# Performance work log

Measured on AMD Instinct MI355X. Metric: run time of the kernel, lower is better.

## Reference

```python
import jax, jax.numpy as jnp
import numpy as np

N = 4096
IN_DIM, HID, OUT_DIM = 512, 256, 128
GAMMA = 6.0            # MCP weight truncation: w(y) = max(1 - y/gamma, 0)
LAM_HAT = 0.9
LAM = 1.0 / LAM_HAT - 1.0
PROP_STEPS = 10


def setup_inputs() -> dict:
    key = jax.random.key(0)
    k_a, k_f, k_w1, k_b1, k_w2, k_b2 = jax.random.split(key, 6)
    p = 32.0 / N  # avg degree ~32
    U = jax.random.uniform(k_a, (N, N))
    A = (U < p).astype(jnp.float32)
    A = jnp.maximum(A, A.T)                       # symmetric
    A = A * (1.0 - jnp.eye(N, dtype=jnp.float32))  # zero diagonal (loops added in forward)
    F = jax.random.normal(k_f, (N, IN_DIM), dtype=jnp.float32)
    W1 = jax.random.normal(k_w1, (IN_DIM, HID), dtype=jnp.float32) * 0.05
    b1 = jax.random.normal(k_b1, (HID,), dtype=jnp.float32) * 0.01
    W2 = jax.random.normal(k_w2, (HID, OUT_DIM), dtype=jnp.float32) * 0.05
    b2 = jax.random.normal(k_b2, (OUT_DIM,), dtype=jnp.float32) * 0.01
    return {"A": A, "F": F, "W1": W1, "b1": b1, "W2": W2, "b2": b2}


def reference(A, F, W1, b1, W2, b2):
    n = A.shape[0]
    # MLP (eval mode: dropout off)
    F0 = jnp.maximum(F @ W1 + b1, 0.0) @ W2 + b2          # [N, out_dim]
    # add self loops
    A = A + jnp.eye(n, dtype=A.dtype)
    D = A.sum(-1)                                          # [N]
    D_sq = jnp.sqrt(D)[:, None]                            # [N,1]
    A_t = A / (D_sq * D_sq.T)                              # sym-normalized adjacency
    diag = jnp.arange(n)
    Fc = F0
    for _ in range(PROP_STEPS):
        X = Fc / D_sq                                      # [N, d]
        sq = jnp.sum(X * X, axis=-1)                       # [N]
        Z = sq[:, None] + sq[None, :] - 2.0 * (X @ X.T)    # pairwise squared dist [N,N]
        Z = jax.lax.stop_gradient(jnp.maximum(Z, 0.0))
        Wm = jnp.maximum(1.0 - jnp.sqrt(Z) / GAMMA, 0.0)   # MCP IRLS weight
        Wm = Wm.at[diag, diag].set(0.0)
        Wm = jnp.where(jnp.isnan(Wm), 1.0, Wm)
        # quasi-Newton IRLS step
        Q = ((Wm * A).sum(-1) / D + LAM)[:, None]          # [N,1]
        Fc = (Wm * A_t) @ Fc / Q + LAM * F0 / Q
    return Fc
```

## Files before the change

kernel.cpp:

```cpp
#include <hip/hip_runtime.h>

#define NN 4096
#define IN_DIM 512
#define HID 256
#define OUT_DIM 128
#define MAXDEG 192
#define INV_GAMMA (1.0f / 6.0f)
#define LAM 0.11111111111111116f
#define PROP_STEPS 10

__global__ void k_analyze(const float* __restrict__ A, unsigned short* __restrict__ cols,
                          int* __restrict__ deg, float* __restrict__ DsqInv,
                          float* __restrict__ Dinv) {
    int wid = threadIdx.x >> 6, lane = threadIdx.x & 63;
    int row = blockIdx.x * 4 + wid;
    const float4* Ar = (const float4*)(A + (size_t)row * NN);
    unsigned short* crow = cols + (size_t)row * MAXDEG;
    int cnt = 0;
    float fsum = 0.f;
    for (int it = 0; it < NN / 256; ++it) {
        float4 v = Ar[it * 64 + lane];
        fsum += (v.x + v.y) + (v.z + v.w);
        int colbase = (it * 64 + lane) * 4;
        float comp[4] = {v.x, v.y, v.z, v.w};
#pragma unroll
        for (int c = 0; c < 4; ++c) {
            bool nz = (comp[c] != 0.f);
            unsigned long long m = __ballot(nz);
            if (nz) {
                int off = cnt + __popcll(m & ((1ull << lane) - 1ull));
                if (off < MAXDEG) crow[off] = (unsigned short)(colbase + c);
            }
            cnt += __popcll(m);
        }
    }
#pragma unroll
    for (int m = 1; m < 64; m <<= 1) fsum += __shfl_xor(fsum, m);
    if (lane == 0) {
        float D = fsum + 1.0f;
        deg[row] = cnt < MAXDEG ? cnt : MAXDEG;
        DsqInv[row] = 1.0f / sqrtf(D);
        Dinv[row] = 1.0f / D;
    }
}

__global__ __launch_bounds__(256) void k_mlp(const float* __restrict__ F,
                      const float* __restrict__ W1, const float* __restrict__ b1,
                      const float* __restrict__ W2, const float* __restrict__ b2,
                      const float* __restrict__ DsqInv,
                      float* __restrict__ F0, float* __restrict__ X0) {
    __shared__ __align__(16) float sF[8 * IN_DIM];
    __shared__ __align__(16) float sW[32 * 256];
    __shared__ __align__(16) float sH[8 * HID];
    int r0 = blockIdx.x * 8;
    int t = threadIdx.x;
#pragma unroll
    for (int i = 0; i < 4; ++i) {
        int idx = i * 256 + t;
        int r = idx >> 7, q = idx & 127;
        *(float4*)&sF[r * IN_DIM + 4 * q] = *(const float4*)&F[(size_t)(r0 + r) * IN_DIM + 4 * q];
    }
    {
        int cq = t & 63, rg = t >> 6;
        float4 accA = make_float4(0.f, 0.f, 0.f, 0.f);
        float4 accB = make_float4(0.f, 0.f, 0.f, 0.f);
        for (int kt = 0; kt < IN_DIM / 32; ++kt) {
            __syncthreads();
#pragma unroll
            for (int i = 0; i < 8; ++i) {
                int idx = i * 256 + t;
                int kr = idx >> 6, q = idx & 63;
                *(float4*)&sW[kr * 256 + 4 * q] =
                    *(const float4*)&W1[(size_t)(kt * 32 + kr) * HID + 4 * q];
            }
            __syncthreads();
#pragma unroll
            for (int kk = 0; kk < 32; ++kk) {
                int k = kt * 32 + kk;
                float4 w = *(float4*)&sW[kk * 256 + 4 * cq];
                float fa = sF[(2 * rg) * IN_DIM + k];
                float fb = sF[(2 * rg + 1) * IN_DIM + k];
                accA.x = fmaf(fa, w.x, accA.x); accA.y = fmaf(fa, w.y, accA.y);
                accA.z = fmaf(fa, w.z, accA.z); accA.w = fmaf(fa, w.w, accA.w);
                accB.x = fmaf(fb, w.x, accB.x); accB.y = fmaf(fb, w.y, accB.y);
                accB.z = fmaf(fb, w.z, accB.z); accB.w = fmaf(fb, w.w, accB.w);
            }
        }
        float4 b = *(const float4*)&b1[4 * cq];
        float4 ha, hb;
        ha.x = fmaxf(accA.x + b.x, 0.f); ha.y = fmaxf(accA.y + b.y, 0.f);
        ha.z = fmaxf(accA.z + b.z, 0.f); ha.w = fmaxf(accA.w + b.w, 0.f);
        hb.x = fmaxf(accB.x + b.x, 0.f); hb.y = fmaxf(accB.y + b.y, 0.f);
        hb.z = fmaxf(accB.z + b.z, 0.f); hb.w = fmaxf(accB.w + b.w, 0.f);
        *(float4*)&sH[(2 * rg) * HID + 4 * cq] = ha;
        *(float4*)&sH[(2 * rg + 1) * HID + 4 * cq] = hb;
    }
    {
        int c = t & 127, half = t >> 7;
        float acc2[4] = {0.f, 0.f, 0.f, 0.f};
        for (int kt = 0; kt < HID / 32; ++kt) {
            __syncthreads();
#pragma unroll
            for (int i = 0; i < 4; ++i) {
                int idx = i * 256 + t;
                int kr = idx >> 5, q = idx & 31;
                *(float4*)&sW[kr * 128 + 4 * q] =
                    *(const float4*)&W2[(size_t)(kt * 32 + kr) * OUT_DIM + 4 * q];
            }
            __syncthreads();
#pragma unroll
            for (int kk = 0; kk < 32; ++kk) {
                int k = kt * 32 + kk;
                float w = sW[kk * 128 + c];
#pragma unroll
                for (int r = 0; r < 4; ++r)
                    acc2[r] = fmaf(sH[(half * 4 + r) * HID + k], w, acc2[r]);
            }
        }
        float b = b2[c];
#pragma unroll
        for (int r = 0; r < 4; ++r) {
            int row = r0 + half * 4 + r;
            float v = acc2[r] + b;
            F0[(size_t)row * OUT_DIM + c] = v;
            X0[(size_t)row * OUT_DIM + c] = v * DsqInv[row];
        }
    }
}

__global__ __launch_bounds__(256) void k_prop(const float* __restrict__ X,
                       const float* __restrict__ F0,
                       const unsigned short* __restrict__ cols, const int* __restrict__ deg,
                       const float* __restrict__ DsqInv, const float* __restrict__ Dinv,
                       float* __restrict__ Xout, float* __restrict__ FcOut, int final_step) {
    __shared__ unsigned short sCols[4][MAXDEG];
    int wid = threadIdx.x >> 6, lane = threadIdx.x & 63;
    int row = blockIdx.x * 4 + wid;
    int g = lane >> 3, oc = lane & 7;
    int dg = deg[row];
    float dsi = DsqInv[row], di = Dinv[row];
    for (int e = lane; e < dg; e += 64) sCols[wid][e] = cols[(size_t)row * MAXDEG + e];
    const float4* Xi4 = (const float4*)(X + (size_t)row * 128 + oc * 16);
    float4 xi0 = Xi4[0], xi1 = Xi4[1], xi2 = Xi4[2], xi3 = Xi4[3];
    float sqi;
    {
        float s = 0.f;
        s = fmaf(xi0.x, xi0.x, s); s = fmaf(xi0.y, xi0.y, s);
        s = fmaf(xi0.z, xi0.z, s); s = fmaf(xi0.w, xi0.w, s);
        s = fmaf(xi1.x, xi1.x, s); s = fmaf(xi1.y, xi1.y, s);
        s = fmaf(xi1.z, xi1.z, s); s = fmaf(xi1.w, xi1.w, s);
        s = fmaf(xi2.x, xi2.x, s); s = fmaf(xi2.y, xi2.y, s);
        s = fmaf(xi2.z, xi2.z, s); s = fmaf(xi2.w, xi2.w, s);
        s = fmaf(xi3.x, xi3.x, s); s = fmaf(xi3.y, xi3.y, s);
        s = fmaf(xi3.z, xi3.z, s); s = fmaf(xi3.w, xi3.w, s);
        s += __shfl_xor(s, 1); s += __shfl_xor(s, 2); s += __shfl_xor(s, 4);
        sqi = s;
    }
    float acc[16];
#pragma unroll
    for (int i = 0; i < 16; ++i) acc[i] = 0.f;
    float qacc = 0.f;
    int nch = (dg + 7) >> 3;
    for (int ch = 0; ch < nch; ++ch) {
        int e = ch * 8 + g;
        bool act = (e < dg);
        int ec = act ? e : (dg - 1);
        int j = (int)sCols[wid][ec];
        const float4* Xj4 = (const float4*)(X + (size_t)j * 128 + oc * 16);
        float4 a = Xj4[0], b = Xj4[1], c = Xj4[2], d = Xj4[3];
        float p = 0.f, sj = 0.f;
        p = fmaf(xi0.x, a.x, p); sj = fmaf(a.x, a.x, sj);
        p = fmaf(xi0.y, a.y, p); sj = fmaf(a.y, a.y, sj);
        p = fmaf(xi0.z, a.z, p); sj = fmaf(a.z, a.z, sj);
        p = fmaf(xi0.w, a.w, p); sj = fmaf(a.w, a.w, sj);
        p = fmaf(xi1.x, b.x, p); sj = fmaf(b.x, b.x, sj);
        p = fmaf(xi1.y, b.y, p); sj = fmaf(b.y, b.y, sj);
        p = fmaf(xi1.z, b.z, p); sj = fmaf(b.z, b.z, sj);
        p = fmaf(xi1.w, b.w, p); sj = fmaf(b.w, b.w, sj);
        p = fmaf(xi2.x, c.x, p); sj = fmaf(c.x, c.x, sj);
        p = fmaf(xi2.y, c.y, p); sj = fmaf(c.y, c.y, sj);
        p = fmaf(xi2.z, c.z, p); sj = fmaf(c.z, c.z, sj);
        p = fmaf(xi2.w, c.w, p); sj = fmaf(c.w, c.w, sj);
        p = fmaf(xi3.x, d.x, p); sj = fmaf(d.x, d.x, sj);
        p = fmaf(xi3.y, d.y, p); sj = fmaf(d.y, d.y, sj);
        p = fmaf(xi3.z, d.z, p); sj = fmaf(d.z, d.z, sj);
        p = fmaf(xi3.w, d.w, p); sj = fmaf(d.w, d.w, sj);
        p += __shfl_xor(p, 1); p += __shfl_xor(p, 2); p += __shfl_xor(p, 4);
        sj += __shfl_xor(sj, 1); sj += __shfl_xor(sj, 2); sj += __shfl_xor(sj, 4);
        float z = fmaxf(sqi + sj - 2.f * p, 0.f);
        float w = fmaxf(1.f - sqrtf(z) * INV_GAMMA, 0.f);
        w = act ? w : 0.f;
        qacc += w;
        acc[0]  = fmaf(w, a.x, acc[0]);  acc[1]  = fmaf(w, a.y, acc[1]);
        acc[2]  = fmaf(w, a.z, acc[2]);  acc[3]  = fmaf(w, a.w, acc[3]);
        acc[4]  = fmaf(w, b.x, acc[4]);  acc[5]  = fmaf(w, b.y, acc[5]);
        acc[6]  = fmaf(w, b.z, acc[6]);  acc[7]  = fmaf(w, b.w, acc[7]);
        acc[8]  = fmaf(w, c.x, acc[8]);  acc[9]  = fmaf(w, c.y, acc[9]);
        acc[10] = fmaf(w, c.z, acc[10]); acc[11] = fmaf(w, c.w, acc[11]);
        acc[12] = fmaf(w, d.x, acc[12]); acc[13] = fmaf(w, d.y, acc[13]);
        acc[14] = fmaf(w, d.z, acc[14]); acc[15] = fmaf(w, d.w, acc[15]);
    }
#pragma unroll
    for (int m = 8; m <= 32; m <<= 1) {
        qacc += __shfl_xor(qacc, m);
#pragma unroll
        for (int i = 0; i < 16; ++i) acc[i] += __shfl_xor(acc[i], m);
    }
    float invQ = 1.f / (qacc * di + LAM);
    if (g == 0) {
        const float4* F04 = (const float4*)(F0 + (size_t)row * 128 + oc * 16);
        float* dstF = (float*)(FcOut + (size_t)row * 128 + oc * 16);
        float* dstX = (float*)(Xout + (size_t)row * 128 + oc * 16);
#pragma unroll
        for (int q = 0; q < 4; ++q) {
            float4 f0 = F04[q];
            float4 o;
            o.x = (dsi * acc[4 * q + 0] + LAM * f0.x) * invQ;
            o.y = (dsi * acc[4 * q + 1] + LAM * f0.y) * invQ;
            o.z = (dsi * acc[4 * q + 2] + LAM * f0.z) * invQ;
            o.w = (dsi * acc[4 * q + 3] + LAM * f0.w) * invQ;
            if (final_step) {
                *(float4*)&dstF[4 * q] = o;
            } else {
                float4 xo;
                xo.x = o.x * dsi; xo.y = o.y * dsi; xo.z = o.z * dsi; xo.w = o.w * dsi;
                *(float4*)&dstX[4 * q] = xo;
            }
        }
    }
}

extern "C" void kernel_launch(void* const* d_in, const int* in_sizes, int n_in,
                              void* d_out, int out_size, void* d_ws, size_t ws_size,
                              hipStream_t stream) {
    const float *A = nullptr, *F = nullptr, *W1 = nullptr, *b1 = nullptr,
                *W2 = nullptr, *b2 = nullptr;
    for (int i = 0; i < n_in; i++) {
        switch (in_sizes[i]) {
            case NN * NN:        A  = (const float*)d_in[i]; break;
            case NN * IN_DIM:    F  = (const float*)d_in[i]; break;
            case IN_DIM * HID:   W1 = (const float*)d_in[i]; break;
            case HID:            b1 = (const float*)d_in[i]; break;
            case HID * OUT_DIM:  W2 = (const float*)d_in[i]; break;
            case OUT_DIM:        b2 = (const float*)d_in[i]; break;
            default: break;
        }
    }
    float* out = (float*)d_out;

    char* ws = (char*)d_ws;
    float* F0     = (float*)ws; ws += (size_t)NN * OUT_DIM * 4;
    float* XA     = (float*)ws; ws += (size_t)NN * OUT_DIM * 4;
    float* XB     = (float*)ws; ws += (size_t)NN * OUT_DIM * 4;
    float* DsqInv = (float*)ws; ws += (size_t)NN * 4;
    float* Dinv   = (float*)ws; ws += (size_t)NN * 4;
    int*   deg    = (int*)ws;   ws += (size_t)NN * 4;
    unsigned short* cols = (unsigned short*)ws; ws += (size_t)NN * MAXDEG * 2;

    hipLaunchKernelGGL(k_analyze, dim3(NN / 4), dim3(256), 0, stream, A, cols, deg, DsqInv, Dinv);
    hipLaunchKernelGGL(k_mlp, dim3(NN / 8), dim3(256), 0, stream,
                       F, W1, b1, W2, b2, DsqInv, F0, XA);

    float* Xc = XA; float* Xn = XB;
    for (int step = 0; step < PROP_STEPS; step++) {
        int fin = (step == PROP_STEPS - 1) ? 1 : 0;
        hipLaunchKernelGGL(k_prop, dim3(NN / 4), dim3(256), 0, stream,
                           Xc, F0, cols, deg, DsqInv, Dinv, Xn, out, fin);
        float* t1 = Xc; Xc = Xn; Xn = t1;
    }
}
```

Measured before the change: 289.8 us.

## Retile MLP with register-prefetched weights and remap prop lanes with gather prefetch

```diff
diff --git a/kernel.cpp b/kernel.cpp
--- a/kernel.cpp
+++ b/kernel.cpp
@@ -49,86 +49,139 @@
                       const float* __restrict__ W2, const float* __restrict__ b2,
                       const float* __restrict__ DsqInv,
                       float* __restrict__ F0, float* __restrict__ X0) {
-    __shared__ __align__(16) float sF[8 * IN_DIM];
+    __shared__ __align__(16) float sF[16 * IN_DIM];
     __shared__ __align__(16) float sW[32 * 256];
-    __shared__ __align__(16) float sH[8 * HID];
-    int r0 = blockIdx.x * 8;
+    __shared__ float sHT[HID * 18];
     int t = threadIdx.x;
-#pragma unroll
-    for (int i = 0; i < 4; ++i) {
+    int r0 = blockIdx.x * 16;
+    const float4* F4 = (const float4*)F;
+    const float4* W1_4 = (const float4*)W1;
+    const float4* W2_4 = (const float4*)W2;
+    float4* sF4 = (float4*)sF;
+    float4* sW4 = (float4*)sW;
+
+#pragma unroll
+    for (int i = 0; i < 8; ++i) {
         int idx = i * 256 + t;
         int r = idx >> 7, q = idx & 127;
-        *(float4*)&sF[r * IN_DIM + 4 * q] = *(const float4*)&F[(size_t)(r0 + r) * IN_DIM + 4 * q];
+        sF4[r * 128 + q] = F4[(size_t)(r0 + r) * 128 + q];
+    }
+    float4 wreg[8];
+#pragma unroll
+    for (int i = 0; i < 8; ++i) {
+        int idx = i * 256 + t;
+        int kr = idx >> 6, q = idx & 63;
+        wreg[i] = W1_4[(size_t)kr * 64 + q];
     }
     {
         int cq = t & 63, rg = t >> 6;
-        float4 accA = make_float4(0.f, 0.f, 0.f, 0.f);
-        float4 accB = make_float4(0.f, 0.f, 0.f, 0.f);
+        float4 acc[4];
+#pragma unroll
+        for (int j = 0; j < 4; ++j) acc[j] = make_float4(0.f, 0.f, 0.f, 0.f);
         for (int kt = 0; kt < IN_DIM / 32; ++kt) {
             __syncthreads();
 #pragma unroll
             for (int i = 0; i < 8; ++i) {
                 int idx = i * 256 + t;
                 int kr = idx >> 6, q = idx & 63;
-                *(float4*)&sW[kr * 256 + 4 * q] =
-                    *(const float4*)&W1[(size_t)(kt * 32 + kr) * HID + 4 * q];
+                sW4[kr * 64 + q] = wreg[i];
             }
             __syncthreads();
-#pragma unroll
-            for (int kk = 0; kk < 32; ++kk) {
-                int k = kt * 32 + kk;
-                float4 w = *(float4*)&sW[kk * 256 + 4 * cq];
-                float fa = sF[(2 * rg) * IN_DIM + k];
-                float fb = sF[(2 * rg + 1) * IN_DIM + k];
-                accA.x = fmaf(fa, w.x, accA.x); accA.y = fmaf(fa, w.y, accA.y);
-                accA.z = fmaf(fa, w.z, accA.z); accA.w = fmaf(fa, w.w, accA.w);
-                accB.x = fmaf(fb, w.x, accB.x); accB.y = fmaf(fb, w.y, accB.y);
-                accB.z = fmaf(fb, w.z, accB.z); accB.w = fmaf(fb, w.w, accB.w);
+            if (kt < IN_DIM / 32 - 1) {
+#pragma unroll
+                for (int i = 0; i < 8; ++i) {
+                    int idx = i * 256 + t;
+                    int kr = idx >> 6, q = idx & 63;
+                    wreg[i] = W1_4[(size_t)((kt + 1) * 32 + kr) * 64 + q];
+                }
+            }
+#pragma unroll
+            for (int g4 = 0; g4 < 8; ++g4) {
+                float4 w0 = sW4[(4 * g4 + 0) * 64 + cq];
+                float4 w1 = sW4[(4 * g4 + 1) * 64 + cq];
+                float4 w2 = sW4[(4 * g4 + 2) * 64 + cq];
+                float4 w3 = sW4[(4 * g4 + 3) * 64 + cq];
+#pragma unroll
+                for (int j = 0; j < 4; ++j) {
+                    float4 f = sF4[(4 * rg + j) * 128 + kt * 8 + g4];
+                    acc[j].x = fmaf(f.x, w0.x, acc[j].x); acc[j].y = fmaf(f.x, w0.y, acc[j].y);
+                    acc[j].z = fmaf(f.x, w0.z, acc[j].z); acc[j].w = fmaf(f.x, w0.w, acc[j].w);
+                    acc[j].x = fmaf(f.y, w1.x, acc[j].x); acc[j].y = fmaf(f.y, w1.y, acc[j].y);
+                    acc[j].z = fmaf(f.y, w1.z, acc[j].z); acc[j].w = fmaf(f.y, w1.w, acc[j].w);
+                    acc[j].x = fmaf(f.z, w2.x, acc[j].x); acc[j].y = fmaf(f.z, w2.y, acc[j].y);
+                    acc[j].z = fmaf(f.z, w2.z, acc[j].z); acc[j].w = fmaf(f.z, w2.w, acc[j].w);
+                    acc[j].x = fmaf(f.w, w3.x, acc[j].x); acc[j].y = fmaf(f.w, w3.y, acc[j].y);
+                    acc[j].z = fmaf(f.w, w3.z, acc[j].z); acc[j].w = fmaf(f.w, w3.w, acc[j].w);
+                }
             }
         }
         float4 b = *(const float4*)&b1[4 * cq];
-        float4 ha, hb;
-        ha.x = fmaxf(accA.x + b.x, 0.f); ha.y = fmaxf(accA.y + b.y, 0.f);
-        ha.z = fmaxf(accA.z + b.z, 0.f); ha.w = fmaxf(accA.w + b.w, 0.f);
-        hb.x = fmaxf(accB.x + b.x, 0.f); hb.y = fmaxf(accB.y + b.y, 0.f);
-        hb.z = fmaxf(accB.z + b.z, 0.f); hb.w = fmaxf(accB.w + b.w, 0.f);
-        *(float4*)&sH[(2 * rg) * HID + 4 * cq] = ha;
-        *(float4*)&sH[(2 * rg + 1) * HID + 4 * cq] = hb;
+#pragma unroll
+        for (int j = 0; j < 4; ++j) {
+            float hx = fmaxf(acc[j].x + b.x, 0.f);
+            float hy = fmaxf(acc[j].y + b.y, 0.f);
+            float hz = fmaxf(acc[j].z + b.z, 0.f);
+            float hw = fmaxf(acc[j].w + b.w, 0.f);
+            int r = 4 * rg + j;
+            sHT[(4 * cq + 0) * 18 + r] = hx;
+            sHT[(4 * cq + 1) * 18 + r] = hy;
+            sHT[(4 * cq + 2) * 18 + r] = hz;
+            sHT[(4 * cq + 3) * 18 + r] = hw;
+        }
+    }
+#pragma unroll
+    for (int i = 0; i < 4; ++i) {
+        int idx = i * 256 + t;
+        int kr = idx >> 5, q = idx & 31;
+        wreg[i] = W2_4[(size_t)kr * 32 + q];
     }
     {
-        int c = t & 127, half = t >> 7;
-        float acc2[4] = {0.f, 0.f, 0.f, 0.f};
+        int cq2 = t & 31, rg2 = t >> 5;
+        float4 accA = make_float4(0.f, 0.f, 0.f, 0.f);
+        float4 accB = make_float4(0.f, 0.f, 0.f, 0.f);
         for (int kt = 0; kt < HID / 32; ++kt) {
             __syncthreads();
 #pragma unroll
             for (int i = 0; i < 4; ++i) {
                 int idx = i * 256 + t;
                 int kr = idx >> 5, q = idx & 31;
-                *(float4*)&sW[kr * 128 + 4 * q] =
-                    *(const float4*)&W2[(size_t)(kt * 32 + kr) * OUT_DIM + 4 * q];
+                sW4[kr * 32 + q] = wreg[i];
             }
             __syncthreads();
+            if (kt < HID / 32 - 1) {
+#pragma unroll
+                for (int i = 0; i < 4; ++i) {
+                    int idx = i * 256 + t;
+                    int kr = idx >> 5, q = idx & 31;
+                    wreg[i] = W2_4[(size_t)((kt + 1) * 32 + kr) * 32 + q];
+                }
+            }
 #pragma unroll
             for (int kk = 0; kk < 32; ++kk) {
-                int k = kt * 32 + kk;
-                float w = sW[kk * 128 + c];
-#pragma unroll
-                for (int r = 0; r < 4; ++r)
-                    acc2[r] = fmaf(sH[(half * 4 + r) * HID + k], w, acc2[r]);
-            }
-        }
-        float b = b2[c];
-#pragma unroll
-        for (int r = 0; r < 4; ++r) {
-            int row = r0 + half * 4 + r;
-            float v = acc2[r] + b;
-            F0[(size_t)row * OUT_DIM + c] = v;
-            X0[(size_t)row * OUT_DIM + c] = v * DsqInv[row];
-        }
+                float4 w = sW4[kk * 32 + cq2];
+                float2 f = *(const float2*)&sHT[(kt * 32 + kk) * 18 + 2 * rg2];
+                accA.x = fmaf(f.x, w.x, accA.x); accA.y = fmaf(f.x, w.y, accA.y);
+                accA.z = fmaf(f.x, w.z, accA.z); accA.w = fmaf(f.x, w.w, accA.w);
+                accB.x = fmaf(f.y, w.x, accB.x); accB.y = fmaf(f.y, w.y, accB.y);
+                accB.z = fmaf(f.y, w.z, accB.z); accB.w = fmaf(f.y, w.w, accB.w);
+            }
+        }
+        float4 b = *(const float4*)&b2[4 * cq2];
+        int rowA = r0 + 2 * rg2, rowB = rowA + 1;
+        float dsA = DsqInv[rowA], dsB = DsqInv[rowB];
+        float4 oA, oB, xA, xB;
+        oA.x = accA.x + b.x; oA.y = accA.y + b.y; oA.z = accA.z + b.z; oA.w = accA.w + b.w;
+        oB.x = accB.x + b.x; oB.y = accB.y + b.y; oB.z = accB.z + b.z; oB.w = accB.w + b.w;
+        xA.x = oA.x * dsA; xA.y = oA.y * dsA; xA.z = oA.z * dsA; xA.w = oA.w * dsA;
+        xB.x = oB.x * dsB; xB.y = oB.y * dsB; xB.z = oB.z * dsB; xB.w = oB.w * dsB;
+        ((float4*)F0)[(size_t)rowA * 32 + cq2] = oA;
+        ((float4*)F0)[(size_t)rowB * 32 + cq2] = oB;
+        ((float4*)X0)[(size_t)rowA * 32 + cq2] = xA;
+        ((float4*)X0)[(size_t)rowB * 32 + cq2] = xB;
     }
 }
 
-__global__ __launch_bounds__(256) void k_prop(const float* __restrict__ X,
+__global__ __launch_bounds__(256, 4) void k_prop(const float* __restrict__ X,
                        const float* __restrict__ F0,
                        const unsigned short* __restrict__ cols, const int* __restrict__ deg,
                        const float* __restrict__ DsqInv, const float* __restrict__ Dinv,
@@ -136,96 +189,93 @@
     __shared__ unsigned short sCols[4][MAXDEG];
     int wid = threadIdx.x >> 6, lane = threadIdx.x & 63;
     int row = blockIdx.x * 4 + wid;
-    int g = lane >> 3, oc = lane & 7;
+    int g = lane >> 4, oc = lane & 15;
     int dg = deg[row];
     float dsi = DsqInv[row], di = Dinv[row];
     for (int e = lane; e < dg; e += 64) sCols[wid][e] = cols[(size_t)row * MAXDEG + e];
-    const float4* Xi4 = (const float4*)(X + (size_t)row * 128 + oc * 16);
-    float4 xi0 = Xi4[0], xi1 = Xi4[1], xi2 = Xi4[2], xi3 = Xi4[3];
+
+    const float4* Xr = (const float4*)(X + (size_t)row * 128);
+    float4 xiA = Xr[oc], xiB = Xr[16 + oc];
     float sqi;
     {
         float s = 0.f;
-        s = fmaf(xi0.x, xi0.x, s); s = fmaf(xi0.y, xi0.y, s);
-        s = fmaf(xi0.z, xi0.z, s); s = fmaf(xi0.w, xi0.w, s);
-        s = fmaf(xi1.x, xi1.x, s); s = fmaf(xi1.y, xi1.y, s);
-        s = fmaf(xi1.z, xi1.z, s); s = fmaf(xi1.w, xi1.w, s);
-        s = fmaf(xi2.x, xi2.x, s); s = fmaf(xi2.y, xi2.y, s);
-        s = fmaf(xi2.z, xi2.z, s); s = fmaf(xi2.w, xi2.w, s);
-        s = fmaf(xi3.x, xi3.x, s); s = fmaf(xi3.y, xi3.y, s);
-        s = fmaf(xi3.z, xi3.z, s); s = fmaf(xi3.w, xi3.w, s);
-        s += __shfl_xor(s, 1); s += __shfl_xor(s, 2); s += __shfl_xor(s, 4);
+        s = fmaf(xiA.x, xiA.x, s); s = fmaf(xiA.y, xiA.y, s);
+        s = fmaf(xiA.z, xiA.z, s); s = fmaf(xiA.w, xiA.w, s);
+        s = fmaf(xiB.x, xiB.x, s); s = fmaf(xiB.y, xiB.y, s);
+        s = fmaf(xiB.z, xiB.z, s); s = fmaf(xiB.w, xiB.w, s);
+        s += __shfl_xor(s, 1); s += __shfl_xor(s, 2);
+        s += __shfl_xor(s, 4); s += __shfl_xor(s, 8);
         sqi = s;
     }
-    float acc[16];
-#pragma unroll
-    for (int i = 0; i < 16; ++i) acc[i] = 0.f;
+    float4 accA = make_float4(0.f, 0.f, 0.f, 0.f);
+    float4 accB = make_float4(0.f, 0.f, 0.f, 0.f);
     float qacc = 0.f;
-    int nch = (dg + 7) >> 3;
-    for (int ch = 0; ch < nch; ++ch) {
-        int e = ch * 8 + g;
-        bool act = (e < dg);
-        int ec = act ? e : (dg - 1);
-        int j = (int)sCols[wid][ec];
-        const float4* Xj4 = (const float4*)(X + (size_t)j * 128 + oc * 16);
-        float4 a = Xj4[0], b = Xj4[1], c = Xj4[2], d = Xj4[3];
-        float p = 0.f, sj = 0.f;
-        p = fmaf(xi0.x, a.x, p); sj = fmaf(a.x, a.x, sj);
-        p = fmaf(xi0.y, a.y, p); sj = fmaf(a.y, a.y, sj);
-        p = fmaf(xi0.z, a.z, p); sj = fmaf(a.z, a.z, sj);
-        p = fmaf(xi0.w, a.w, p); sj = fmaf(a.w, a.w, sj);
-        p = fmaf(xi1.x, b.x, p); sj = fmaf(b.x, b.x, sj);
-        p = fmaf(xi1.y, b.y, p); sj = fmaf(b.y, b.y, sj);
-        p = fmaf(xi1.z, b.z, p); sj = fmaf(b.z, b.z, sj);
-        p = fmaf(xi1.w, b.w, p); sj = fmaf(b.w, b.w, sj);
-        p = fmaf(xi2.x, c.x, p); sj = fmaf(c.x, c.x, sj);
-        p = fmaf(xi2.y, c.y, p); sj = fmaf(c.y, c.y, sj);
-        p = fmaf(xi2.z, c.z, p); sj = fmaf(c.z, c.z, sj);
-        p = fmaf(xi2.w, c.w, p); sj = fmaf(c.w, c.w, sj);
-        p = fmaf(xi3.x, d.x, p); sj = fmaf(d.x, d.x, sj);
-        p = fmaf(xi3.y, d.y, p); sj = fmaf(d.y, d.y, sj);
-        p = fmaf(xi3.z, d.z, p); sj = fmaf(d.z, d.z, sj);
-        p = fmaf(xi3.w, d.w, p); sj = fmaf(d.w, d.w, sj);
-        p += __shfl_xor(p, 1); p += __shfl_xor(p, 2); p += __shfl_xor(p, 4);
-        sj += __shfl_xor(sj, 1); sj += __shfl_xor(sj, 2); sj += __shfl_xor(sj, 4);
-        float z = fmaxf(sqi + sj - 2.f * p, 0.f);
-        float w = fmaxf(1.f - sqrtf(z) * INV_GAMMA, 0.f);
-        w = act ? w : 0.f;
-        qacc += w;
-        acc[0]  = fmaf(w, a.x, acc[0]);  acc[1]  = fmaf(w, a.y, acc[1]);
-        acc[2]  = fmaf(w, a.z, acc[2]);  acc[3]  = fmaf(w, a.w, acc[3]);
-        acc[4]  = fmaf(w, b.x, acc[4]);  acc[5]  = fmaf(w, b.y, acc[5]);
-        acc[6]  = fmaf(w, b.z, acc[6]);  acc[7]  = fmaf(w, b.w, acc[7]);
-        acc[8]  = fmaf(w, c.x, acc[8]);  acc[9]  = fmaf(w, c.y, acc[9]);
-        acc[10] = fmaf(w, c.z, acc[10]); acc[11] = fmaf(w, c.w, acc[11]);
-        acc[12] = fmaf(w, d.x, acc[12]); acc[13] = fmaf(w, d.y, acc[13]);
-        acc[14] = fmaf(w, d.z, acc[14]); acc[15] = fmaf(w, d.w, acc[15]);
-    }
-#pragma unroll
-    for (int m = 8; m <= 32; m <<= 1) {
+    if (dg > 0) {
+        int nch = (dg + 3) >> 2;
+        int e0 = (g < dg) ? g : (dg - 1);
+        int j0 = (int)sCols[wid][e0];
+        const float4* Xj = (const float4*)(X + (size_t)j0 * 128);
+        float4 cA = Xj[oc], cB = Xj[16 + oc];
+        for (int ch = 0; ch < nch; ++ch) {
+            int en = (ch + 1) * 4 + g; en = (en < dg) ? en : (dg - 1);
+            int jn = (int)sCols[wid][en];
+            const float4* Xn = (const float4*)(X + (size_t)jn * 128);
+            float4 nA = Xn[oc], nB = Xn[16 + oc];
+            float p = 0.f, sj = 0.f;
+            p = fmaf(xiA.x, cA.x, p); sj = fmaf(cA.x, cA.x, sj);
+            p = fmaf(xiA.y, cA.y, p); sj = fmaf(cA.y, cA.y, sj);
+            p = fmaf(xiA.z, cA.z, p); sj = fmaf(cA.z, cA.z, sj);
+            p = fmaf(xiA.w, cA.w, p); sj = fmaf(cA.w, cA.w, sj);
+            p = fmaf(xiB.x, cB.x, p); sj = fmaf(cB.x, cB.x, sj);
+            p = fmaf(xiB.y, cB.y, p); sj = fmaf(cB.y, cB.y, sj);
+            p = fmaf(xiB.z, cB.z, p); sj = fmaf(cB.z, cB.z, sj);
+            p = fmaf(xiB.w, cB.w, p); sj = fmaf(cB.w, cB.w, sj);
+            p += __shfl_xor(p, 1); sj += __shfl_xor(sj, 1);
+            p += __shfl_xor(p, 2); sj += __shfl_xor(sj, 2);
+            p += __shfl_xor(p, 4); sj += __shfl_xor(sj, 4);
+            p += __shfl_xor(p, 8); sj += __shfl_xor(sj, 8);
+            float z = fmaxf(sqi + sj - 2.f * p, 0.f);
+            float w = fmaxf(1.f - sqrtf(z) * INV_GAMMA, 0.f);
+            bool act = (ch * 4 + g) < dg;
+            w = act ? w : 0.f;
+            qacc += w;
+            accA.x = fmaf(w, cA.x, accA.x); accA.y = fmaf(w, cA.y, accA.y);
+            accA.z = fmaf(w, cA.z, accA.z); accA.w = fmaf(w, cA.w, accA.w);
+            accB.x = fmaf(w, cB.x, accB.x); accB.y = fmaf(w, cB.y, accB.y);
+            accB.z = fmaf(w, cB.z, accB.z); accB.w = fmaf(w, cB.w, accB.w);
+            cA = nA; cB = nB;
+        }
+    }
+#pragma unroll
+    for (int m = 16; m <= 32; m <<= 1) {
         qacc += __shfl_xor(qacc, m);
-#pragma unroll
-        for (int i = 0; i < 16; ++i) acc[i] += __shfl_xor(acc[i], m);
+        accA.x += __shfl_xor(accA.x, m); accA.y += __shfl_xor(accA.y, m);
+        accA.z += __shfl_xor(accA.z, m); accA.w += __shfl_xor(accA.w, m);
+        accB.x += __shfl_xor(accB.x, m); accB.y += __shfl_xor(accB.y, m);
+        accB.z += __shfl_xor(accB.z, m); accB.w += __shfl_xor(accB.w, m);
     }
     float invQ = 1.f / (qacc * di + LAM);
     if (g == 0) {
-        const float4* F04 = (const float4*)(F0 + (size_t)row * 128 + oc * 16);
-        float* dstF = (float*)(FcOut + (size_t)row * 128 + oc * 16);
-        float* dstX = (float*)(Xout + (size_t)row * 128 + oc * 16);
-#pragma unroll
-        for (int q = 0; q < 4; ++q) {
-            float4 f0 = F04[q];
-            float4 o;
-            o.x = (dsi * acc[4 * q + 0] + LAM * f0.x) * invQ;
-            o.y = (dsi * acc[4 * q + 1] + LAM * f0.y) * invQ;
-            o.z = (dsi * acc[4 * q + 2] + LAM * f0.z) * invQ;
-            o.w = (dsi * acc[4 * q + 3] + LAM * f0.w) * invQ;
-            if (final_step) {
-                *(float4*)&dstF[4 * q] = o;
-            } else {
-                float4 xo;
-                xo.x = o.x * dsi; xo.y = o.y * dsi; xo.z = o.z * dsi; xo.w = o.w * dsi;
-                *(float4*)&dstX[4 * q] = xo;
-            }
+        const float4* F04 = (const float4*)(F0 + (size_t)row * 128);
+        float4 f0A = F04[oc], f0B = F04[16 + oc];
+        float4 oA, oB;
+        oA.x = (dsi * accA.x + LAM * f0A.x) * invQ;
+        oA.y = (dsi * accA.y + LAM * f0A.y) * invQ;
+        oA.z = (dsi * accA.z + LAM * f0A.z) * invQ;
+        oA.w = (dsi * accA.w + LAM * f0A.w) * invQ;
+        oB.x = (dsi * accB.x + LAM * f0B.x) * invQ;
+        oB.y = (dsi * accB.y + LAM * f0B.y) * invQ;
+        oB.z = (dsi * accB.z + LAM * f0B.z) * invQ;
+        oB.w = (dsi * accB.w + LAM * f0B.w) * invQ;
+        if (final_step) {
+            float4* dst = (float4*)(FcOut + (size_t)row * 128);
+            dst[oc] = oA; dst[16 + oc] = oB;
+        } else {
+            float4 xA, xB;
+            xA.x = oA.x * dsi; xA.y = oA.y * dsi; xA.z = oA.z * dsi; xA.w = oA.w * dsi;
+            xB.x = oB.x * dsi; xB.y = oB.y * dsi; xB.z = oB.z * dsi; xB.w = oB.w * dsi;
+            float4* dst = (float4*)(Xout + (size_t)row * 128);
+            dst[oc] = xA; dst[16 + oc] = xB;
         }
     }
 }
@@ -258,7 +308,7 @@
     unsigned short* cols = (unsigned short*)ws; ws += (size_t)NN * MAXDEG * 2;
 
     hipLaunchKernelGGL(k_analyze, dim3(NN / 4), dim3(256), 0, stream, A, cols, deg, DsqInv, Dinv);
-    hipLaunchKernelGGL(k_mlp, dim3(NN / 8), dim3(256), 0, stream,
+    hipLaunchKernelGGL(k_mlp, dim3(NN / 16), dim3(256), 0, stream,
                        F, W1, b1, W2, b2, DsqInv, F0, XA);
 
     float* Xc = XA; float* Xn = XB;
```

Result: slower. 345.9 us (+19.4%).
